# Kernel tuning notes

Hardware: AMD Instinct MI355X
Metric: run time of the kernel (lower is better)

The kernel has to match this reference:

```python
import jax, jax.numpy as jnp
import numpy as np

I_DIM = 20000        # item (node) count; emb_mat has I_DIM+1 rows
EMB_DIM = 128        # input embedding dim
D_DIM = 128          # hidden (scaled) dim
N_EDGES = 640000     # number of (src, dst) edges


def setup_inputs() -> dict:
    key = jax.random.key(0)
    k1, k2, k3, k4 = jax.random.split(key, 4)
    emb_mat = jax.random.normal(k1, (I_DIM + 1, EMB_DIM), dtype=jnp.float32)
    # edges must be sorted by source node (column 0) so that the original
    # tf.repeat(segment_sums, bincount(src)) trick is well-defined.
    edge = jax.random.randint(k2, (N_EDGES, 2), 0, I_DIM + 1, dtype=jnp.int64)
    order = jnp.argsort(edge[:, 0])
    edge = edge[order]
    W_scale = jax.random.normal(k3, (EMB_DIM, D_DIM), dtype=jnp.float32) * 0.05
    b_scale = jnp.zeros((D_DIM,), dtype=jnp.float32)
    W_att = jax.random.normal(k4, (2 * D_DIM, 1), dtype=jnp.float32) * 0.05
    b_att = jnp.zeros((1,), dtype=jnp.float32)
    return {"emb_mat": emb_mat, "edge": edge, "W_scale": W_scale,
            "b_scale": b_scale, "W_att": W_att, "b_att": b_att}


def reference(emb_mat, edge, W_scale, b_scale, W_att, b_att):
    num_segments = emb_mat.shape[0]          # i_dim + 1
    seg = edge[:, 0]                         # source nodes (segment ids), [E]

    # gather both endpoints, scale: [E, 2, emb] -> [E, 2, d]
    edge_emb = emb_mat[edge] @ W_scale + b_scale
    E = edge_emb.shape[0]
    # attention logit per edge from concatenated endpoint features
    att = (edge_emb.reshape(E, -1) @ W_att + b_att)[:, 0]   # [E]
    att = jax.nn.leaky_relu(att, negative_slope=0.2)
    scores = jnp.exp(att - 1.0)                              # exp(att - ones)

    # manual segment softmax over edges grouped by source node
    score_sum = jax.ops.segment_sum(scores, seg, num_segments=num_segments)
    score_norm = scores / score_sum[seg]                     # [E]

    # scale all node embeddings once, gather destination features
    item_scaled = emb_mat @ W_scale + b_scale                # [N, d]
    items = item_scaled[edge[:, 1]]                          # [E, d]

    agg = jax.ops.segment_sum(score_norm[:, None] * items, seg,
                              num_segments=num_segments)     # [N, d]
    return jax.nn.sigmoid(agg)
```

## Files before the change

kernel.cpp:

```cpp
#include <hip/hip_runtime.h>
#include <math.h>

#define NSEG 20001
#define EMB  128
#define NE   640000

#define SCALE_BLOCKS 313
#define BOUNDS_BLOCKS 2500
#define LDSL 129

__device__ __forceinline__ float dot4(float4 a, float4 b) {
    return a.x*b.x + a.y*b.y + a.z*b.z + a.w*b.w;
}

#define FMA4(acc, s, b) { acc.x += (s)*(b).x; acc.y += (s)*(b).y; acc.z += (s)*(b).z; acc.w += (s)*(b).w; }

__device__ __forceinline__ unsigned f2bf(float x) {
    unsigned u = __float_as_uint(x);
    return (u + 0x7fffu + ((u >> 16) & 1u)) >> 16;
}

__global__ __launch_bounds__(256) void prep_kernel(
    const float* __restrict__ emb, const float* __restrict__ W,
    const float* __restrict__ bsc, const float* __restrict__ Watt,
    const int* __restrict__ edge,
    unsigned short* __restrict__ tab,
    float* __restrict__ a_src, float* __restrict__ a_dst,
    int* __restrict__ seg_start, int* __restrict__ dst)
{
    const int tid = threadIdx.x;
    if (blockIdx.x >= SCALE_BLOCKS) {
        int e = (blockIdx.x - SCALE_BLOCKS) * 256 + tid;
        int2 p = ((const int2*)edge)[e];
        dst[e] = p.y;
        int sp = __shfl_up(p.x, 1);
        if ((tid & 63) == 0) sp = (e == 0) ? -1 : edge[2*e - 2];
        for (int t = sp + 1; t <= p.x; ++t) seg_start[t] = e;
        if (e == NE - 1) {
            for (int t = p.x + 1; t <= NSEG; ++t) seg_start[t] = NE;
        }
        return;
    }

    __shared__ float emb_s[64 * LDSL];
    const int r0 = blockIdx.x * 64;

    const float4* embg4 = (const float4*)emb;
    const int gmax = NSEG * 32 - 1;
    #pragma unroll
    for (int j = 0; j < 8; ++j) {
        int idx = tid + j * 256;
        int row = idx >> 5, f4 = idx & 31;
        int g = r0 * 32 + idx;
        float4 v = embg4[g <= gmax ? g : gmax];
        float* p = &emb_s[row * LDSL + f4 * 4];
        p[0] = v.x; p[1] = v.y; p[2] = v.z; p[3] = v.w;
    }
    __syncthreads();

    const int cg   = tid & 15;
    const int rowb = (tid >> 4) * 4;

    float4 accA[4] = {{0,0,0,0},{0,0,0,0},{0,0,0,0},{0,0,0,0}};
    float4 accB[4] = {{0,0,0,0},{0,0,0,0},{0,0,0,0},{0,0,0,0}};
    const float4* Wg4 = (const float4*)W;

    #pragma unroll 4
    for (int k = 0; k < EMB; ++k) {
        float4 w0 = Wg4[k*32 + cg*2];
        float4 w1 = Wg4[k*32 + cg*2 + 1];
        float a0 = emb_s[(rowb+0)*LDSL + k];
        float a1 = emb_s[(rowb+1)*LDSL + k];
        float a2 = emb_s[(rowb+2)*LDSL + k];
        float a3 = emb_s[(rowb+3)*LDSL + k];
        FMA4(accA[0], a0, w0); FMA4(accB[0], a0, w1);
        FMA4(accA[1], a1, w0); FMA4(accB[1], a1, w1);
        FMA4(accA[2], a2, w0); FMA4(accB[2], a2, w1);
        FMA4(accA[3], a3, w0); FMA4(accB[3], a3, w1);
    }

    const float4 bsA = *(const float4*)&bsc[cg*8];
    const float4 bsB = *(const float4*)&bsc[cg*8 + 4];
    const float4 wsA = *(const float4*)&Watt[cg*8];
    const float4 wsB = *(const float4*)&Watt[cg*8 + 4];
    const float4 wdA = *(const float4*)&Watt[EMB + cg*8];
    const float4 wdB = *(const float4*)&Watt[EMB + cg*8 + 4];

    #pragma unroll
    for (int r = 0; r < 4; ++r) {
        float4 A = accA[r], B = accB[r];
        A.x += bsA.x; A.y += bsA.y; A.z += bsA.z; A.w += bsA.w;
        B.x += bsB.x; B.y += bsB.y; B.z += bsB.z; B.w += bsB.w;
        const int row = r0 + rowb + r;

        if (row < NSEG) {
            uint4 pkt;
            pkt.x = f2bf(A.x) | (f2bf(A.y) << 16);
            pkt.y = f2bf(A.z) | (f2bf(A.w) << 16);
            pkt.z = f2bf(B.x) | (f2bf(B.y) << 16);
            pkt.w = f2bf(B.z) | (f2bf(B.w) << 16);
            ((uint4*)tab)[row * 16 + cg] = pkt;
        }

        float ps = dot4(A, wsA) + dot4(B, wsB);
        float pd = dot4(A, wdA) + dot4(B, wdB);
        #pragma unroll
        for (int off = 8; off >= 1; off >>= 1) {
            ps += __shfl_xor(ps, off);
            pd += __shfl_xor(pd, off);
        }
        if (cg == 0 && row < NSEG) { a_src[row] = ps; a_dst[row] = pd; }
    }
}

__device__ __forceinline__ float bf_lo(unsigned u) { return __uint_as_float(u << 16); }
__device__ __forceinline__ float bf_hi(unsigned u) { return __uint_as_float(u & 0xffff0000u); }
__device__ __forceinline__ float bcastf(float v, int j) {
    return __uint_as_float(__builtin_amdgcn_readlane(__float_as_uint(v), j));
}

__global__ __launch_bounds__(256) void agg_kernel(
    const int* __restrict__ dst, const float* __restrict__ a_src,
    const float* __restrict__ a_dst, const float* __restrict__ b_att,
    const int* __restrict__ seg_start, const unsigned int* __restrict__ tab32,
    float* __restrict__ out)
{
    const int wid = blockIdx.x * 4 + (threadIdx.x >> 6);
    if (wid >= NSEG) return;
    const int lane = threadIdx.x & 63;
    const unsigned int* tabl = tab32 + lane;

    const int s0 = seg_start[wid];
    const int s1 = seg_start[wid + 1];
    const float aS = a_src[wid] + b_att[0];

    float accx = 0.f, accy = 0.f, ssum = 0.f;

    for (int cb = s0; cb < s1; cb += 64) {
        int n = s1 - cb; if (n > 64) n = 64;
        int e = cb + lane;
        int dmine = 0; float sc = 0.f;
        if (lane < n) {
            dmine = dst[e] << 6;
            float att = aS + a_dst[dmine >> 6];
            att = att > 0.f ? att : 0.2f * att;
            sc  = expf(att - 1.f);
        }
        ssum += sc;

        int j = 0;
        for (; j + 7 < n; j += 8) {
            float w0 = bcastf(sc, j+0), w1 = bcastf(sc, j+1);
            float w2 = bcastf(sc, j+2), w3 = bcastf(sc, j+3);
            float w4 = bcastf(sc, j+4), w5 = bcastf(sc, j+5);
            float w6 = bcastf(sc, j+6), w7 = bcastf(sc, j+7);
            int d0 = __builtin_amdgcn_readlane(dmine, j+0);
            int d1 = __builtin_amdgcn_readlane(dmine, j+1);
            int d2 = __builtin_amdgcn_readlane(dmine, j+2);
            int d3 = __builtin_amdgcn_readlane(dmine, j+3);
            int d4 = __builtin_amdgcn_readlane(dmine, j+4);
            int d5 = __builtin_amdgcn_readlane(dmine, j+5);
            int d6 = __builtin_amdgcn_readlane(dmine, j+6);
            int d7 = __builtin_amdgcn_readlane(dmine, j+7);
            unsigned u0 = tabl[d0], u1 = tabl[d1], u2 = tabl[d2], u3 = tabl[d3];
            unsigned u4 = tabl[d4], u5 = tabl[d5], u6 = tabl[d6], u7 = tabl[d7];
            accx += w0 * bf_lo(u0); accy += w0 * bf_hi(u0);
            accx += w1 * bf_lo(u1); accy += w1 * bf_hi(u1);
            accx += w2 * bf_lo(u2); accy += w2 * bf_hi(u2);
            accx += w3 * bf_lo(u3); accy += w3 * bf_hi(u3);
            accx += w4 * bf_lo(u4); accy += w4 * bf_hi(u4);
            accx += w5 * bf_lo(u5); accy += w5 * bf_hi(u5);
            accx += w6 * bf_lo(u6); accy += w6 * bf_hi(u6);
            accx += w7 * bf_lo(u7); accy += w7 * bf_hi(u7);
        }
        for (; j < n; ++j) {
            float w = bcastf(sc, j);
            int   d = __builtin_amdgcn_readlane(dmine, j);
            unsigned u = tabl[d];
            accx += w * bf_lo(u);
            accy += w * bf_hi(u);
        }
    }

    #pragma unroll
    for (int off = 32; off >= 1; off >>= 1) ssum += __shfl_xor(ssum, off);

    const float inv = (s1 > s0) ? 1.f / ssum : 0.f;
    float ox = accx * inv, oy = accy * inv;
    ox = 1.f / (1.f + expf(-ox));
    oy = 1.f / (1.f + expf(-oy));
    *(float2*)&out[wid * EMB + 2 * lane] = make_float2(ox, oy);
}

extern "C" void kernel_launch(void* const* d_in, const int* in_sizes, int n_in,
                              void* d_out, int out_size, void* d_ws, size_t ws_size,
                              hipStream_t stream) {
    const float* emb  = (const float*)d_in[0];
    const int*   edge = (const int*)  d_in[1];
    const float* W    = (const float*)d_in[2];
    const float* bsc  = (const float*)d_in[3];
    const float* Watt = (const float*)d_in[4];
    const float* batt = (const float*)d_in[5];
    float* out = (float*)d_out;

    unsigned short* tab = (unsigned short*)d_ws;
    float* a_src = (float*)(tab + (size_t)NSEG * EMB);
    float* a_dst = a_src + NSEG;
    int*   seg_start = (int*)(a_dst + NSEG);
    int*   dstc = seg_start + NSEG + 3;

    prep_kernel<<<SCALE_BLOCKS + BOUNDS_BLOCKS, 256, 0, stream>>>(
        emb, W, bsc, Watt, edge, tab, a_src, a_dst, seg_start, dstc);
    agg_kernel<<<(NSEG + 3) / 4, 256, 0, stream>>>(
        dstc, a_src, a_dst, batt, seg_start, (const unsigned int*)tab, out);
}
```

Before: 111.4 us.

## Split aggregation feature dimension across two blocks, half-waves process alternating edges

Each segment is now handled by two blocks, each covering half of the 128 feature columns. Within a wave, the two 32-lane halves process even and odd edges at the same time and combine their partial sums with a cross-half shuffle before the sigmoid. This doubles the wave count and exposes more independent gathers per wave, to help hide gather latency. In exchange, each segment's score computation (a_dst loads, exp) is done twice, and the grid has twice as many blocks.

```diff
diff --git a/kernel.cpp b/kernel.cpp
--- a/kernel.cpp
+++ b/kernel.cpp
@@ -125,10 +125,13 @@
     const int* __restrict__ seg_start, const unsigned int* __restrict__ tab32,
     float* __restrict__ out)
 {
-    const int wid = blockIdx.x * 4 + (threadIdx.x >> 6);
+    const int half = blockIdx.x & 1;
+    const int wid  = (blockIdx.x >> 1) * 4 + (threadIdx.x >> 6);
     if (wid >= NSEG) return;
     const int lane = threadIdx.x & 63;
-    const unsigned int* tabl = tab32 + lane;
+    const int sub  = lane >> 5;
+    const int dw   = lane & 31;
+    const unsigned int* tabl = tab32 + half * 32 + dw;
 
     const int s0 = seg_start[wid];
     const int s1 = seg_start[wid + 1];
@@ -149,33 +152,30 @@
         ssum += sc;
 
         int j = 0;
-        for (; j + 7 < n; j += 8) {
-            float w0 = bcastf(sc, j+0), w1 = bcastf(sc, j+1);
-            float w2 = bcastf(sc, j+2), w3 = bcastf(sc, j+3);
-            float w4 = bcastf(sc, j+4), w5 = bcastf(sc, j+5);
-            float w6 = bcastf(sc, j+6), w7 = bcastf(sc, j+7);
-            int d0 = __builtin_amdgcn_readlane(dmine, j+0);
-            int d1 = __builtin_amdgcn_readlane(dmine, j+1);
-            int d2 = __builtin_amdgcn_readlane(dmine, j+2);
-            int d3 = __builtin_amdgcn_readlane(dmine, j+3);
-            int d4 = __builtin_amdgcn_readlane(dmine, j+4);
-            int d5 = __builtin_amdgcn_readlane(dmine, j+5);
-            int d6 = __builtin_amdgcn_readlane(dmine, j+6);
-            int d7 = __builtin_amdgcn_readlane(dmine, j+7);
-            unsigned u0 = tabl[d0], u1 = tabl[d1], u2 = tabl[d2], u3 = tabl[d3];
-            unsigned u4 = tabl[d4], u5 = tabl[d5], u6 = tabl[d6], u7 = tabl[d7];
-            accx += w0 * bf_lo(u0); accy += w0 * bf_hi(u0);
-            accx += w1 * bf_lo(u1); accy += w1 * bf_hi(u1);
-            accx += w2 * bf_lo(u2); accy += w2 * bf_hi(u2);
-            accx += w3 * bf_lo(u3); accy += w3 * bf_hi(u3);
-            accx += w4 * bf_lo(u4); accy += w4 * bf_hi(u4);
-            accx += w5 * bf_lo(u5); accy += w5 * bf_hi(u5);
-            accx += w6 * bf_lo(u6); accy += w6 * bf_hi(u6);
-            accx += w7 * bf_lo(u7); accy += w7 * bf_hi(u7);
-        }
-        for (; j < n; ++j) {
-            float w = bcastf(sc, j);
-            int   d = __builtin_amdgcn_readlane(dmine, j);
+        for (; j + 15 < n; j += 16) {
+            #pragma unroll
+            for (int p = 0; p < 8; ++p) {
+                float wa = bcastf(sc, j + 2*p);
+                float wb = bcastf(sc, j + 2*p + 1);
+                int   da = __builtin_amdgcn_readlane(dmine, j + 2*p);
+                int   db = __builtin_amdgcn_readlane(dmine, j + 2*p + 1);
+                float w = sub ? wb : wa;
+                int   d = sub ? db : da;
+                unsigned u = tabl[d];
+                accx += w * bf_lo(u);
+                accy += w * bf_hi(u);
+            }
+        }
+        for (; j < n; j += 2) {
+            float wa = bcastf(sc, j);
+            int   da = __builtin_amdgcn_readlane(dmine, j);
+            float wb = 0.f; int db = da;
+            if (j + 1 < n) {
+                wb = bcastf(sc, j + 1);
+                db = __builtin_amdgcn_readlane(dmine, j + 1);
+            }
+            float w = sub ? wb : wa;
+            int   d = sub ? db : da;
             unsigned u = tabl[d];
             accx += w * bf_lo(u);
             accy += w * bf_hi(u);
@@ -185,11 +185,15 @@
     #pragma unroll
     for (int off = 32; off >= 1; off >>= 1) ssum += __shfl_xor(ssum, off);
 
+    accx += __shfl_xor(accx, 32);
+    accy += __shfl_xor(accy, 32);
+
     const float inv = (s1 > s0) ? 1.f / ssum : 0.f;
-    float ox = accx * inv, oy = accy * inv;
-    ox = 1.f / (1.f + expf(-ox));
-    oy = 1.f / (1.f + expf(-oy));
-    *(float2*)&out[wid * EMB + 2 * lane] = make_float2(ox, oy);
+    if (lane < 32) {
+        float ox = 1.f / (1.f + expf(-accx * inv));
+        float oy = 1.f / (1.f + expf(-accy * inv));
+        *(float2*)&out[wid * EMB + half * 64 + 2 * dw] = make_float2(ox, oy);
+    }
 }
 
 extern "C" void kernel_launch(void* const* d_in, const int* in_sizes, int n_in,
@@ -211,6 +215,6 @@
 
     prep_kernel<<<SCALE_BLOCKS + BOUNDS_BLOCKS, 256, 0, stream>>>(
         emb, W, bsc, Watt, edge, tab, a_src, a_dst, seg_start, dstc);
-    agg_kernel<<<(NSEG + 3) / 4, 256, 0, stream>>>(
+    agg_kernel<<<2 * ((NSEG + 3) / 4), 256, 0, stream>>>(
         dstc, a_src, a_dst, batt, seg_start, (const unsigned int*)tab, out);
 }
```

Result: slower. 125.3 us (+12.6%).

## Precompute per-edge scores in separate kernel and pack with dst index

Applied to the files above, without the earlier changes.

Moves the attention-score computation (leaky relu and exp) out of the aggregation kernel into a new per-edge score kernel. That kernel writes an int2 pair holding the pre-shifted destination index and the score. The aggregation loop then loads pairs with uniform addresses instead of computing per-lane scores and broadcasting them via readlane. The score sum is accumulated redundantly per lane, so the wavefront reduction goes away. This adds a third kernel launch and an extra 5 MB write/read of pair data.

```diff
diff --git a/kernel.cpp b/kernel.cpp
--- a/kernel.cpp
+++ b/kernel.cpp
@@ -26,13 +26,12 @@
     const int* __restrict__ edge,
     unsigned short* __restrict__ tab,
     float* __restrict__ a_src, float* __restrict__ a_dst,
-    int* __restrict__ seg_start, int* __restrict__ dst)
+    int* __restrict__ seg_start)
 {
     const int tid = threadIdx.x;
     if (blockIdx.x >= SCALE_BLOCKS) {
         int e = (blockIdx.x - SCALE_BLOCKS) * 256 + tid;
         int2 p = ((const int2*)edge)[e];
-        dst[e] = p.y;
         int sp = __shfl_up(p.x, 1);
         if ((tid & 63) == 0) sp = (e == 0) ? -1 : edge[2*e - 2];
         for (int t = sp + 1; t <= p.x; ++t) seg_start[t] = e;
@@ -113,17 +112,25 @@
     }
 }
 
+__global__ __launch_bounds__(256) void score_kernel(
+    const int* __restrict__ edge, const float* __restrict__ a_src,
+    const float* __restrict__ a_dst, const float* __restrict__ b_att,
+    int2* __restrict__ pair)
+{
+    int e = blockIdx.x * 256 + threadIdx.x;
+    int2 p = ((const int2*)edge)[e];
+    float att = a_src[p.x] + a_dst[p.y] + b_att[0];
+    att = att > 0.f ? att : 0.2f * att;
+    float sc = expf(att - 1.f);
+    pair[e] = make_int2(p.y << 6, __float_as_int(sc));
+}
+
 __device__ __forceinline__ float bf_lo(unsigned u) { return __uint_as_float(u << 16); }
 __device__ __forceinline__ float bf_hi(unsigned u) { return __uint_as_float(u & 0xffff0000u); }
-__device__ __forceinline__ float bcastf(float v, int j) {
-    return __uint_as_float(__builtin_amdgcn_readlane(__float_as_uint(v), j));
-}
 
 __global__ __launch_bounds__(256) void agg_kernel(
-    const int* __restrict__ dst, const float* __restrict__ a_src,
-    const float* __restrict__ a_dst, const float* __restrict__ b_att,
-    const int* __restrict__ seg_start, const unsigned int* __restrict__ tab32,
-    float* __restrict__ out)
+    const int2* __restrict__ pair, const int* __restrict__ seg_start,
+    const unsigned int* __restrict__ tab32, float* __restrict__ out)
 {
     const int wid = blockIdx.x * 4 + (threadIdx.x >> 6);
     if (wid >= NSEG) return;
@@ -132,59 +139,41 @@
 
     const int s0 = seg_start[wid];
     const int s1 = seg_start[wid + 1];
-    const float aS = a_src[wid] + b_att[0];
-
-    float accx = 0.f, accy = 0.f, ssum = 0.f;
-
-    for (int cb = s0; cb < s1; cb += 64) {
-        int n = s1 - cb; if (n > 64) n = 64;
-        int e = cb + lane;
-        int dmine = 0; float sc = 0.f;
-        if (lane < n) {
-            dmine = dst[e] << 6;
-            float att = aS + a_dst[dmine >> 6];
-            att = att > 0.f ? att : 0.2f * att;
-            sc  = expf(att - 1.f);
-        }
-        ssum += sc;
-
-        int j = 0;
-        for (; j + 7 < n; j += 8) {
-            float w0 = bcastf(sc, j+0), w1 = bcastf(sc, j+1);
-            float w2 = bcastf(sc, j+2), w3 = bcastf(sc, j+3);
-            float w4 = bcastf(sc, j+4), w5 = bcastf(sc, j+5);
-            float w6 = bcastf(sc, j+6), w7 = bcastf(sc, j+7);
-            int d0 = __builtin_amdgcn_readlane(dmine, j+0);
-            int d1 = __builtin_amdgcn_readlane(dmine, j+1);
-            int d2 = __builtin_amdgcn_readlane(dmine, j+2);
-            int d3 = __builtin_amdgcn_readlane(dmine, j+3);
-            int d4 = __builtin_amdgcn_readlane(dmine, j+4);
-            int d5 = __builtin_amdgcn_readlane(dmine, j+5);
-            int d6 = __builtin_amdgcn_readlane(dmine, j+6);
-            int d7 = __builtin_amdgcn_readlane(dmine, j+7);
-            unsigned u0 = tabl[d0], u1 = tabl[d1], u2 = tabl[d2], u3 = tabl[d3];
-            unsigned u4 = tabl[d4], u5 = tabl[d5], u6 = tabl[d6], u7 = tabl[d7];
-            accx += w0 * bf_lo(u0); accy += w0 * bf_hi(u0);
-            accx += w1 * bf_lo(u1); accy += w1 * bf_hi(u1);
-            accx += w2 * bf_lo(u2); accy += w2 * bf_hi(u2);
-            accx += w3 * bf_lo(u3); accy += w3 * bf_hi(u3);
-            accx += w4 * bf_lo(u4); accy += w4 * bf_hi(u4);
-            accx += w5 * bf_lo(u5); accy += w5 * bf_hi(u5);
-            accx += w6 * bf_lo(u6); accy += w6 * bf_hi(u6);
-            accx += w7 * bf_lo(u7); accy += w7 * bf_hi(u7);
-        }
-        for (; j < n; ++j) {
-            float w = bcastf(sc, j);
-            int   d = __builtin_amdgcn_readlane(dmine, j);
-            unsigned u = tabl[d];
-            accx += w * bf_lo(u);
-            accy += w * bf_hi(u);
-        }
-    }
-
-    #pragma unroll
-    for (int off = 32; off >= 1; off >>= 1) ssum += __shfl_xor(ssum, off);
-
+
+    float accx = 0.f, accy = 0.f;
+    float ss0 = 0.f, ss1 = 0.f;
+
+    int j = s0;
+    for (; j + 7 < s1; j += 8) {
+        int2 p0 = pair[j+0], p1 = pair[j+1], p2 = pair[j+2], p3 = pair[j+3];
+        int2 p4 = pair[j+4], p5 = pair[j+5], p6 = pair[j+6], p7 = pair[j+7];
+        unsigned u0 = tabl[p0.x], u1 = tabl[p1.x], u2 = tabl[p2.x], u3 = tabl[p3.x];
+        unsigned u4 = tabl[p4.x], u5 = tabl[p5.x], u6 = tabl[p6.x], u7 = tabl[p7.x];
+        float w0 = __int_as_float(p0.y), w1 = __int_as_float(p1.y);
+        float w2 = __int_as_float(p2.y), w3 = __int_as_float(p3.y);
+        float w4 = __int_as_float(p4.y), w5 = __int_as_float(p5.y);
+        float w6 = __int_as_float(p6.y), w7 = __int_as_float(p7.y);
+        ss0 += w0; ss1 += w1; ss0 += w2; ss1 += w3;
+        ss0 += w4; ss1 += w5; ss0 += w6; ss1 += w7;
+        accx += w0 * bf_lo(u0); accy += w0 * bf_hi(u0);
+        accx += w1 * bf_lo(u1); accy += w1 * bf_hi(u1);
+        accx += w2 * bf_lo(u2); accy += w2 * bf_hi(u2);
+        accx += w3 * bf_lo(u3); accy += w3 * bf_hi(u3);
+        accx += w4 * bf_lo(u4); accy += w4 * bf_hi(u4);
+        accx += w5 * bf_lo(u5); accy += w5 * bf_hi(u5);
+        accx += w6 * bf_lo(u6); accy += w6 * bf_hi(u6);
+        accx += w7 * bf_lo(u7); accy += w7 * bf_hi(u7);
+    }
+    for (; j < s1; ++j) {
+        int2 p = pair[j];
+        unsigned u = tabl[p.x];
+        float w = __int_as_float(p.y);
+        ss0 += w;
+        accx += w * bf_lo(u);
+        accy += w * bf_hi(u);
+    }
+
+    float ssum = ss0 + ss1;
     const float inv = (s1 > s0) ? 1.f / ssum : 0.f;
     float ox = accx * inv, oy = accy * inv;
     ox = 1.f / (1.f + expf(-ox));
@@ -207,10 +196,11 @@
     float* a_src = (float*)(tab + (size_t)NSEG * EMB);
     float* a_dst = a_src + NSEG;
     int*   seg_start = (int*)(a_dst + NSEG);
-    int*   dstc = seg_start + NSEG + 3;
+    int2*  pair = (int2*)(seg_start + NSEG + 3);
 
     prep_kernel<<<SCALE_BLOCKS + BOUNDS_BLOCKS, 256, 0, stream>>>(
-        emb, W, bsc, Watt, edge, tab, a_src, a_dst, seg_start, dstc);
+        emb, W, bsc, Watt, edge, tab, a_src, a_dst, seg_start);
+    score_kernel<<<NE / 256, 256, 0, stream>>>(edge, a_src, a_dst, batt, pair);
     agg_kernel<<<(NSEG + 3) / 4, 256, 0, stream>>>(
-        dstc, a_src, a_dst, batt, seg_start, (const unsigned int*)tab, out);
-}
+        pair, seg_start, (const unsigned int*)tab, out);
+}
```

Result: slower. 121.0 us (+8.7%).
